# Optimization experiments

Measured on AMD Instinct MI355X. Metric: run time of the kernel, lower is better.

The kernel has to match this reference:

```python
import jax, jax.numpy as jnp
import numpy as np
from jax import lax

DELAY = 4410      # delay_samples
FEEDBACK = 0.5    # feedback


def setup_inputs() -> dict:
    key = jax.random.key(0)
    n = 6000 * DELAY  # 26,460,000 samples, divisible by DELAY
    x = jax.random.normal(key, (n,), dtype=jnp.float32)
    return {"x": x}


def reference(x):
    # Comb-filter recurrence: y[n] = x[n] + feedback * y[n - DELAY],
    # with the first DELAY outputs seeded by a zero buffer.
    # Reshape into [n_chunks, DELAY]; each of the DELAY lanes is an
    # independent first-order IIR over chunks -> single lax.scan.
    xr = x.reshape(-1, DELAY)  # [n_chunks, DELAY]

    def step(carry, xc):
        y = xc + FEEDBACK * carry  # carry = previous output chunk (the buffer)
        return y, y

    _, ys = lax.scan(step, jnp.zeros((DELAY,), x.dtype), xr)
    return ys.reshape(-1)
```

## Files before the change

kernel.cpp:

```cpp
#include <hip/hip_runtime.h>

#define DELAY   4410
#define NPAIR   2205
#define NCHUNK  6000
#define FB      0.5f
#define TCH     60
#define KLOOK   16
#define THREADS 256

typedef float v2f __attribute__((ext_vector_type(2)));

__global__ __launch_bounds__(THREADS)
void ReverbModel_67508295958534_kernel(const float* __restrict__ x,
                                       float* __restrict__ y) {
    int p = blockIdx.x * THREADS + threadIdx.x;
    if (p >= NPAIR) return;
    const int c0 = blockIdx.y * TCH;

    const v2f* __restrict__ x2 = (const v2f*)x;
    v2f* __restrict__ y2 = (v2f*)y;

    float cy0 = 0.0f, cy1 = 0.0f;

    int cstart = c0 - KLOOK;
    if (cstart < 0) cstart = 0;
    #pragma unroll 8
    for (int c = cstart; c < c0; ++c) {
        v2f v = x2[(size_t)c * NPAIR + p];
        cy0 = v.x + FB * cy0;
        cy1 = v.y + FB * cy1;
    }

    const int cend = c0 + TCH;
    #pragma unroll 8
    for (int c = c0; c < cend; ++c) {
        v2f v = x2[(size_t)c * NPAIR + p];
        cy0 = v.x + FB * cy0;
        cy1 = v.y + FB * cy1;
        v2f o; o.x = cy0; o.y = cy1;
        __builtin_nontemporal_store(o, &y2[(size_t)c * NPAIR + p]);
    }
}

extern "C" void kernel_launch(void* const* d_in, const int* in_sizes, int n_in,
                              void* d_out, int out_size, void* d_ws, size_t ws_size,
                              hipStream_t stream) {
    const float* x = (const float*)d_in[0];
    float* y = (float*)d_out;

    dim3 grid((NPAIR + THREADS - 1) / THREADS,
              NCHUNK / TCH);
    dim3 block(THREADS);
    ReverbModel_67508295958534_kernel<<<grid, block, 0, stream>>>(x, y);
}
```

Measured before the change: 44.90 us.

## Have each block cover a full chunk row across all lanes with multiple pairs per thread

The launch becomes a 1D grid over chunk tiles. Each 512-thread block now processes every one of the 2205 lane pairs of its chunk range, with four strided pairs per thread plus a tail pair for the first 157 threads. It also lowers TCH to 24 and KLOOK to 12, and drops the nontemporal store hint. The aim is to cut the wasted threads in the partial last block of the old 2D grid and to give each thread more independent memory operations in flight. In exchange, the warm-up reads become a larger share of the work (12 of every 36 chunks instead of 16 of 76), and the tail branch leaves most threads idle during that step.

Result: slower. 48.61 us (+8.3%).

```diff
diff --git a/kernel.cpp b/kernel.cpp
--- a/kernel.cpp
+++ b/kernel.cpp
@@ -4,41 +4,62 @@
 #define NPAIR   2205
 #define NCHUNK  6000
 #define FB      0.5f
-#define TCH     60
-#define KLOOK   16
-#define THREADS 256
+#define TCH     24
+#define KLOOK   12
+#define THREADS 512
+#define NJ      4
+#define TAILP   157
 
 typedef float v2f __attribute__((ext_vector_type(2)));
 
 __global__ __launch_bounds__(THREADS)
 void ReverbModel_67508295958534_kernel(const float* __restrict__ x,
                                        float* __restrict__ y) {
-    int p = blockIdx.x * THREADS + threadIdx.x;
-    if (p >= NPAIR) return;
-    const int c0 = blockIdx.y * TCH;
-
+    const int t  = threadIdx.x;
+    const int c0 = blockIdx.x * TCH;
     const v2f* __restrict__ x2 = (const v2f*)x;
     v2f* __restrict__ y2 = (v2f*)y;
 
-    float cy0 = 0.0f, cy1 = 0.0f;
+    float ca[NJ + 1][2] = {};
+    const bool tail = (t < TAILP);
 
     int cstart = c0 - KLOOK;
     if (cstart < 0) cstart = 0;
-    #pragma unroll 8
     for (int c = cstart; c < c0; ++c) {
-        v2f v = x2[(size_t)c * NPAIR + p];
-        cy0 = v.x + FB * cy0;
-        cy1 = v.y + FB * cy1;
+        size_t rb = (size_t)c * NPAIR + t;
+        #pragma unroll
+        for (int j = 0; j < NJ; ++j) {
+            v2f v = x2[rb + j * THREADS];
+            ca[j][0] = v.x + FB * ca[j][0];
+            ca[j][1] = v.y + FB * ca[j][1];
+        }
+        if (tail) {
+            v2f v = x2[rb + NJ * THREADS];
+            ca[NJ][0] = v.x + FB * ca[NJ][0];
+            ca[NJ][1] = v.y + FB * ca[NJ][1];
+        }
     }
 
-    const int cend = c0 + TCH;
-    #pragma unroll 8
-    for (int c = c0; c < cend; ++c) {
-        v2f v = x2[(size_t)c * NPAIR + p];
-        cy0 = v.x + FB * cy0;
-        cy1 = v.y + FB * cy1;
-        v2f o; o.x = cy0; o.y = cy1;
-        __builtin_nontemporal_store(o, &y2[(size_t)c * NPAIR + p]);
+    #pragma unroll 2
+    for (int c = c0; c < c0 + TCH; ++c) {
+        size_t rb = (size_t)c * NPAIR + t;
+        #pragma unroll
+        for (int j = 0; j < NJ; ++j) {
+            v2f v = x2[rb + j * THREADS];
+            float o0 = v.x + FB * ca[j][0];
+            float o1 = v.y + FB * ca[j][1];
+            ca[j][0] = o0; ca[j][1] = o1;
+            v2f o; o.x = o0; o.y = o1;
+            y2[rb + j * THREADS] = o;
+        }
+        if (tail) {
+            v2f v = x2[rb + NJ * THREADS];
+            float o0 = v.x + FB * ca[NJ][0];
+            float o1 = v.y + FB * ca[NJ][1];
+            ca[NJ][0] = o0; ca[NJ][1] = o1;
+            v2f o; o.x = o0; o.y = o1;
+            y2[rb + NJ * THREADS] = o;
+        }
     }
 }
 
@@ -48,8 +69,7 @@
     const float* x = (const float*)d_in[0];
     float* y = (float*)d_out;
 
-    dim3 grid((NPAIR + THREADS - 1) / THREADS,
-              NCHUNK / TCH);
+    dim3 grid(NCHUNK / TCH);
     dim3 block(THREADS);
     ReverbModel_67508295958534_kernel<<<grid, block, 0, stream>>>(x, y);
 }
```
